# Optimization experiments

Measured on AMD Instinct MI355X. Metric: run time of the kernel, lower is better.

## Reference

```python
import jax, jax.numpy as jnp
import numpy as np

N = 1024
D_X = 128
D_Y = 128
NUM_STEPS = 200


def setup_inputs() -> dict:
    key = jax.random.key(0)
    k1, k2, k3, k4, k5 = jax.random.split(key, 5)
    init_samples_x = jax.random.normal(k1, (N, D_X), dtype=jnp.float32)
    init_samples_y = jax.random.normal(k2, (N, D_Y), dtype=jnp.float32)
    mean_final = jax.random.normal(k3, (D_X,), dtype=jnp.float32)
    # variance must be positive and bounded away from zero
    var_final = jax.random.uniform(k4, (D_X,), dtype=jnp.float32, minval=0.25, maxval=0.75)
    gammas = jnp.linspace(1e-3, 1e-2, NUM_STEPS, dtype=jnp.float32)
    # pre-generated per-step Gaussian noise (replaces torch.randn inside the loop)
    noise = jax.random.normal(k5, (NUM_STEPS, N, D_X), dtype=jnp.float32)
    return {
        "init_samples_x": init_samples_x,
        "init_samples_y": init_samples_y,
        "mean_final": mean_final,
        "var_final": var_final,
        "gammas": gammas,
        "noise": noise,
    }


def reference(init_samples_x, init_samples_y, mean_final, var_final, gammas, noise):
    """Faithful JAX port of Langevin.record_init_langevin.

    grad_gauss(x, m, v) = -(x - m) / v
    per step k:
        t_old = x + gamma_k * grad_gauss(x)
        x     = t_old + sqrt(2*gamma_k) * z_k
        t_new = x + gamma_k * grad_gauss(x)
        record x, y, t_old - t_new
    """
    num_steps = gammas.shape[0]
    n = init_samples_x.shape[0]

    def step(x, inp):
        gamma, z = inp
        t_old = x + gamma * (-(x - mean_final) / var_final)
        x_new = t_old + jnp.sqrt(2.0 * gamma) * z
        t_new = x_new + gamma * (-(x_new - mean_final) / var_final)
        return x_new, (x_new, t_old - t_new)

    _, (xs, outs) = jax.lax.scan(step, init_samples_x, (gammas, noise))
    # scan stacks along leading (step) axis -> [S, N, D]; match torch layout [N, S, D]
    x_tot = jnp.transpose(xs, (1, 0, 2))
    out = jnp.transpose(outs, (1, 0, 2))
    # y is constant across steps; the torch loop just replicates it
    y_tot = jnp.broadcast_to(init_samples_y[:, None, :], (n, num_steps, init_samples_y.shape[1]))
    steps_expanded = jnp.broadcast_to(
        jnp.arange(num_steps, dtype=jnp.int32)[None, :, None], (n, num_steps, 1)
    )
    return x_tot, y_tot, out, steps_expanded
```

## Files before the change

### kernel.cpp

```cpp
#include <hip/hip_runtime.h>
#include <math.h>

constexpr int N   = 1024;
constexpr int D   = 128;
constexpr int S   = 200;
constexpr int D2  = D / 2;
constexpr int ND2 = N * D2;
constexpr int CHAIN_BLOCKS = (N * D2) / 256;
constexpr int PF  = 8;

typedef float f2 __attribute__((ext_vector_type(2)));
typedef float f4 __attribute__((ext_vector_type(4)));

__global__ __launch_bounds__(256, 4) void langevin_kernel(
    const f2* __restrict__ x0,
    const f4* __restrict__ y0,
    const f2* __restrict__ mean,
    const f2* __restrict__ var,
    const float* __restrict__ gammas,
    const f2* __restrict__ noise,
    f2* __restrict__ x_tot,
    f4* __restrict__ y_tot,
    f2* __restrict__ outp,
    float* __restrict__ steps)
{
    if (blockIdx.x >= CHAIN_BLOCKS) {
        const int n   = blockIdx.x - CHAIN_BLOCKS;
        const int t   = threadIdx.x;
        const int col = t & 31;
        const int r0  = t >> 5;
        const f4  yv  = y0[(size_t)n * 32 + col];
        f4* yq = y_tot + (size_t)n * (S * 32);
        #pragma unroll
        for (int j = 0; j < S / 8; ++j) {
            const int k = r0 + j * 8;
            __builtin_nontemporal_store(yv, &yq[(size_t)k * 32 + col]);
        }
        if (t < S) steps[(size_t)n * S + t] = (float)t;
        return;
    }

    __shared__ float sg[S];
    __shared__ float ss[S];
    for (int i = threadIdx.x; i < S; i += 256) {
        float g = gammas[i];
        sg[i] = g;
        ss[i] = sqrtf(2.0f * g);
    }
    __syncthreads();

    const int idx = blockIdx.x * 256 + threadIdx.x;
    const int n   = idx >> 6;
    const int dp  = idx & 63;

    f2 x        = x0[idx];
    const f2 m  = mean[dp];
    const f2 v  = var[dp];
    const float ivx = 1.0f / v.x;
    const float ivy = 1.0f / v.y;

    const f2* zp = noise + idx;
    f2* xq = x_tot + (size_t)n * (S * D2) + dp;
    f2* oq = outp  + (size_t)n * (S * D2) + dp;

    f2 zb[PF];
    #pragma unroll
    for (int i = 0; i < PF; ++i)
        zb[i] = __builtin_nontemporal_load(&zp[(size_t)i * ND2]);

    #pragma unroll 1
    for (int kb = 0; kb < S; kb += PF) {
        f2 zn[PF];
        if (kb + PF < S) {
            #pragma unroll
            for (int i = 0; i < PF; ++i)
                zn[i] = __builtin_nontemporal_load(&zp[(size_t)(kb + PF + i) * ND2]);
        }
        #pragma unroll
        for (int i = 0; i < PF; ++i) {
            const int k = kb + i;
            const float g = sg[k];
            const float s = ss[k];
            const float gx = g * ivx;
            const float gy = g * ivy;

            const float tox = fmaf(-gx, x.x - m.x, x.x);
            const float toy = fmaf(-gy, x.y - m.y, x.y);
            x.x = fmaf(s, zb[i].x, tox);
            x.y = fmaf(s, zb[i].y, toy);
            const float tnx = fmaf(-gx, x.x - m.x, x.x);
            const float tny = fmaf(-gy, x.y - m.y, x.y);

            f2 o;
            o.x = tox - tnx;
            o.y = toy - tny;

            __builtin_nontemporal_store(x, &xq[(size_t)k * D2]);
            __builtin_nontemporal_store(o, &oq[(size_t)k * D2]);
        }
        #pragma unroll
        for (int i = 0; i < PF; ++i) zb[i] = zn[i];
    }
}

extern "C" void kernel_launch(void* const* d_in, const int* in_sizes, int n_in,
                              void* d_out, int out_size, void* d_ws, size_t ws_size,
                              hipStream_t stream)
{
    const float* x0     = (const float*)d_in[0];
    const float* y0     = (const float*)d_in[1];
    const float* mean   = (const float*)d_in[2];
    const float* var    = (const float*)d_in[3];
    const float* gammas = (const float*)d_in[4];
    const float* noise  = (const float*)d_in[5];

    float* x_tot = (float*)d_out;
    float* y_tot = x_tot + (size_t)N * S * D;
    float* outp  = y_tot + (size_t)N * S * D;
    float* steps = outp  + (size_t)N * S * D;

    dim3 grid(CHAIN_BLOCKS + N);
    dim3 block(256);
    langevin_kernel<<<grid, block, 0, stream>>>(
        (const f2*)x0, (const f4*)y0, (const f2*)mean,
        (const f2*)var, gammas, (const f2*)noise,
        (f2*)x_tot, (f4*)y_tot, (f2*)outp, steps);
}
```

Baseline: 396.6 us.

## Split time recurrence into segments via boundary precompute pass for more parallelism

Adds a first kernel that runs the x recurrence over all steps, reading the noise, and saves the state at seven segment boundaries into workspace. A second kernel then launches eight times as many chain blocks, each replaying one 25-step segment from its boundary state and writing x and the diff output. The aim is to expose more parallelism than the original 256 chain blocks, which run a serial 200-step loop. The cost is an extra kernel launch and a second full read of the noise tensor (about 105 MB). The original single kernel is kept as a fallback when the workspace is too small.

```diff
diff --git a/kernel.cpp b/kernel.cpp
--- a/kernel.cpp
+++ b/kernel.cpp
@@ -7,10 +7,165 @@
 constexpr int D2  = D / 2;
 constexpr int ND2 = N * D2;
 constexpr int CHAIN_BLOCKS = (N * D2) / 256;
+constexpr int SEG = 8;
+constexpr int L   = S / SEG;
+constexpr int PF1 = 10;
+constexpr int PF2 = 5;
 constexpr int PF  = 8;
 
 typedef float f2 __attribute__((ext_vector_type(2)));
 typedef float f4 __attribute__((ext_vector_type(4)));
+
+__global__ __launch_bounds__(256, 4) void boundary_kernel(
+    const f2* __restrict__ x0,
+    const f2* __restrict__ mean,
+    const f2* __restrict__ var,
+    const float* __restrict__ gammas,
+    const f2* __restrict__ noise,
+    f2* __restrict__ bnd)
+{
+    __shared__ float sg[S];
+    __shared__ float ss[S];
+    for (int i = threadIdx.x; i < S; i += 256) {
+        float g = gammas[i];
+        sg[i] = g;
+        ss[i] = sqrtf(2.0f * g);
+    }
+    __syncthreads();
+
+    const int idx = blockIdx.x * 256 + threadIdx.x;
+    const int dp  = idx & 63;
+
+    f2 x        = x0[idx];
+    const f2 m  = mean[dp];
+    const f2 v  = var[dp];
+    const float ivx = 1.0f / v.x;
+    const float ivy = 1.0f / v.y;
+
+    const f2* zp = noise + idx;
+
+    f2 zb[PF1];
+    #pragma unroll
+    for (int i = 0; i < PF1; ++i) zb[i] = zp[(size_t)i * ND2];
+
+    #pragma unroll 1
+    for (int kb = 0; kb < S; kb += PF1) {
+        f2 zn[PF1];
+        if (kb + PF1 < S) {
+            #pragma unroll
+            for (int i = 0; i < PF1; ++i)
+                zn[i] = zp[(size_t)(kb + PF1 + i) * ND2];
+        }
+        #pragma unroll
+        for (int i = 0; i < PF1; ++i) {
+            const int k = kb + i;
+            const float g = sg[k];
+            const float s = ss[k];
+            const float gx = g * ivx;
+            const float gy = g * ivy;
+            x.x = fmaf(s, zb[i].x, fmaf(-gx, x.x - m.x, x.x));
+            x.y = fmaf(s, zb[i].y, fmaf(-gy, x.y - m.y, x.y));
+            if (((k + 1) % L) == 0 && (k + 1) < S)
+                bnd[(size_t)((k + 1) / L - 1) * ND2 + idx] = x;
+        }
+        #pragma unroll
+        for (int i = 0; i < PF1; ++i) zb[i] = zn[i];
+    }
+}
+
+__global__ __launch_bounds__(256, 6) void segment_kernel(
+    const f2* __restrict__ x0,
+    const f4* __restrict__ y0,
+    const f2* __restrict__ mean,
+    const f2* __restrict__ var,
+    const float* __restrict__ gammas,
+    const f2* __restrict__ noise,
+    const f2* __restrict__ bnd,
+    f2* __restrict__ x_tot,
+    f4* __restrict__ y_tot,
+    f2* __restrict__ outp,
+    float* __restrict__ steps)
+{
+    if (blockIdx.x >= SEG * CHAIN_BLOCKS) {
+        const int n   = blockIdx.x - SEG * CHAIN_BLOCKS;
+        const int t   = threadIdx.x;
+        const int col = t & 31;
+        const int r0  = t >> 5;
+        const f4  yv  = y0[(size_t)n * 32 + col];
+        f4* yq = y_tot + (size_t)n * (S * 32);
+        #pragma unroll
+        for (int j = 0; j < S / 8; ++j) {
+            const int k = r0 + j * 8;
+            __builtin_nontemporal_store(yv, &yq[(size_t)k * 32 + col]);
+        }
+        if (t < S) steps[(size_t)n * S + t] = (float)t;
+        return;
+    }
+
+    __shared__ float sg[L];
+    __shared__ float ss[L];
+    const int seg = blockIdx.x / CHAIN_BLOCKS;
+    const int rb  = blockIdx.x % CHAIN_BLOCKS;
+    const int k0  = seg * L;
+    if (threadIdx.x < L) {
+        float g = gammas[k0 + threadIdx.x];
+        sg[threadIdx.x] = g;
+        ss[threadIdx.x] = sqrtf(2.0f * g);
+    }
+    __syncthreads();
+
+    const int idx = rb * 256 + threadIdx.x;
+    const int n   = idx >> 6;
+    const int dp  = idx & 63;
+
+    f2 x = (seg == 0) ? x0[idx] : bnd[(size_t)(seg - 1) * ND2 + idx];
+    const f2 m  = mean[dp];
+    const f2 v  = var[dp];
+    const float ivx = 1.0f / v.x;
+    const float ivy = 1.0f / v.y;
+
+    const f2* zp = noise + (size_t)k0 * ND2 + idx;
+    f2* xq = x_tot + (size_t)n * (S * D2) + (size_t)k0 * D2 + dp;
+    f2* oq = outp  + (size_t)n * (S * D2) + (size_t)k0 * D2 + dp;
+
+    f2 zb[PF2];
+    #pragma unroll
+    for (int i = 0; i < PF2; ++i) zb[i] = zp[(size_t)i * ND2];
+
+    #pragma unroll 1
+    for (int kb = 0; kb < L; kb += PF2) {
+        f2 zn[PF2];
+        if (kb + PF2 < L) {
+            #pragma unroll
+            for (int i = 0; i < PF2; ++i)
+                zn[i] = zp[(size_t)(kb + PF2 + i) * ND2];
+        }
+        #pragma unroll
+        for (int i = 0; i < PF2; ++i) {
+            const int k = kb + i;
+            const float g = sg[k];
+            const float s = ss[k];
+            const float gx = g * ivx;
+            const float gy = g * ivy;
+
+            const float tox = fmaf(-gx, x.x - m.x, x.x);
+            const float toy = fmaf(-gy, x.y - m.y, x.y);
+            x.x = fmaf(s, zb[i].x, tox);
+            x.y = fmaf(s, zb[i].y, toy);
+            const float tnx = fmaf(-gx, x.x - m.x, x.x);
+            const float tny = fmaf(-gy, x.y - m.y, x.y);
+
+            f2 o;
+            o.x = tox - tnx;
+            o.y = toy - tny;
+
+            __builtin_nontemporal_store(x, &xq[(size_t)k * D2]);
+            __builtin_nontemporal_store(o, &oq[(size_t)k * D2]);
+        }
+        #pragma unroll
+        for (int i = 0; i < PF2; ++i) zb[i] = zn[i];
+    }
+}
 
 __global__ __launch_bounds__(256, 4) void langevin_kernel(
     const f2* __restrict__ x0,
@@ -119,10 +274,19 @@
     float* outp  = y_tot + (size_t)N * S * D;
     float* steps = outp  + (size_t)N * S * D;
 
-    dim3 grid(CHAIN_BLOCKS + N);
-    dim3 block(256);
-    langevin_kernel<<<grid, block, 0, stream>>>(
-        (const f2*)x0, (const f4*)y0, (const f2*)mean,
-        (const f2*)var, gammas, (const f2*)noise,
-        (f2*)x_tot, (f4*)y_tot, (f2*)outp, steps);
-}
+    const size_t need = (size_t)(SEG - 1) * ND2 * sizeof(f2);
+    if (d_ws != nullptr && ws_size >= need) {
+        boundary_kernel<<<CHAIN_BLOCKS, 256, 0, stream>>>(
+            (const f2*)x0, (const f2*)mean, (const f2*)var, gammas,
+            (const f2*)noise, (f2*)d_ws);
+        segment_kernel<<<SEG * CHAIN_BLOCKS + N, 256, 0, stream>>>(
+            (const f2*)x0, (const f4*)y0, (const f2*)mean, (const f2*)var,
+            gammas, (const f2*)noise, (const f2*)d_ws,
+            (f2*)x_tot, (f4*)y_tot, (f2*)outp, steps);
+    } else {
+        langevin_kernel<<<CHAIN_BLOCKS + N, 256, 0, stream>>>(
+            (const f2*)x0, (const f4*)y0, (const f2*)mean, (const f2*)var,
+            gammas, (const f2*)noise,
+            (f2*)x_tot, (f4*)y_tot, (f2*)outp, steps);
+    }
+}
```

Result: no change. 399.6 us (+0.8%).

## Split Langevin chains into time segments with recomputed prefixes

Applied to the files above, without the earlier changes.

Each chain is split into 8 time segments handled by separate blocks. Each block replays the earlier steps, reading their noise without writing, to rebuild its starting state, then emits its own 25 steps. This raises the number of blocks working on the serial recurrence so the latency of one long chain no longer dominates. In exchange, total noise reads grow several-fold. Occupancy hint and prefetch depth are also changed.

```diff
diff --git a/kernel.cpp b/kernel.cpp
--- a/kernel.cpp
+++ b/kernel.cpp
@@ -7,12 +7,14 @@
 constexpr int D2  = D / 2;
 constexpr int ND2 = N * D2;
 constexpr int CHAIN_BLOCKS = (N * D2) / 256;
-constexpr int PF  = 8;
+constexpr int SEG = 8;
+constexpr int L   = S / SEG;
+constexpr int PF  = 5;
 
 typedef float f2 __attribute__((ext_vector_type(2)));
 typedef float f4 __attribute__((ext_vector_type(4)));
 
-__global__ __launch_bounds__(256, 4) void langevin_kernel(
+__global__ __launch_bounds__(256, 6) void langevin_seg_kernel(
     const f2* __restrict__ x0,
     const f4* __restrict__ y0,
     const f2* __restrict__ mean,
@@ -24,8 +26,8 @@
     f2* __restrict__ outp,
     float* __restrict__ steps)
 {
-    if (blockIdx.x >= CHAIN_BLOCKS) {
-        const int n   = blockIdx.x - CHAIN_BLOCKS;
+    if (blockIdx.x >= SEG * CHAIN_BLOCKS) {
+        const int n   = blockIdx.x - SEG * CHAIN_BLOCKS;
         const int t   = threadIdx.x;
         const int col = t & 31;
         const int r0  = t >> 5;
@@ -49,7 +51,11 @@
     }
     __syncthreads();
 
-    const int idx = blockIdx.x * 256 + threadIdx.x;
+    const int seg = blockIdx.x / CHAIN_BLOCKS;
+    const int rb  = blockIdx.x % CHAIN_BLOCKS;
+    const int k0  = seg * L;
+
+    const int idx = rb * 256 + threadIdx.x;
     const int n   = idx >> 6;
     const int dp  = idx & 63;
 
@@ -60,25 +66,47 @@
     const float ivy = 1.0f / v.y;
 
     const f2* zp = noise + idx;
-    f2* xq = x_tot + (size_t)n * (S * D2) + dp;
-    f2* oq = outp  + (size_t)n * (S * D2) + dp;
 
     f2 zb[PF];
     #pragma unroll
-    for (int i = 0; i < PF; ++i)
-        zb[i] = __builtin_nontemporal_load(&zp[(size_t)i * ND2]);
+    for (int i = 0; i < PF; ++i) zb[i] = zp[(size_t)i * ND2];
 
     #pragma unroll 1
-    for (int kb = 0; kb < S; kb += PF) {
+    for (int kb = 0; kb < k0; kb += PF) {
         f2 zn[PF];
-        if (kb + PF < S) {
-            #pragma unroll
-            for (int i = 0; i < PF; ++i)
-                zn[i] = __builtin_nontemporal_load(&zp[(size_t)(kb + PF + i) * ND2]);
-        }
+        #pragma unroll
+        for (int i = 0; i < PF; ++i)
+            zn[i] = zp[(size_t)(kb + PF + i) * ND2];
         #pragma unroll
         for (int i = 0; i < PF; ++i) {
             const int k = kb + i;
+            const float g = sg[k];
+            const float s = ss[k];
+            const float gx = g * ivx;
+            const float gy = g * ivy;
+            const float tox = fmaf(-gx, x.x - m.x, x.x);
+            const float toy = fmaf(-gy, x.y - m.y, x.y);
+            x.x = fmaf(s, zb[i].x, tox);
+            x.y = fmaf(s, zb[i].y, toy);
+        }
+        #pragma unroll
+        for (int i = 0; i < PF; ++i) zb[i] = zn[i];
+    }
+
+    const f2* zq = zp + (size_t)k0 * ND2;
+    f2* xq = x_tot + (size_t)n * (S * D2) + (size_t)k0 * D2 + dp;
+    f2* oq = outp  + (size_t)n * (S * D2) + (size_t)k0 * D2 + dp;
+
+    #pragma unroll 1
+    for (int kb = 0; kb < L; kb += PF) {
+        f2 zn[PF];
+        const bool more = (k0 + kb + PF) < S;
+        #pragma unroll
+        for (int i = 0; i < PF; ++i)
+            zn[i] = more ? zq[(size_t)(kb + PF + i) * ND2] : zb[i];
+        #pragma unroll
+        for (int i = 0; i < PF; ++i) {
+            const int k = k0 + kb + i;
             const float g = sg[k];
             const float s = ss[k];
             const float gx = g * ivx;
@@ -95,8 +123,8 @@
             o.x = tox - tnx;
             o.y = toy - tny;
 
-            __builtin_nontemporal_store(x, &xq[(size_t)k * D2]);
-            __builtin_nontemporal_store(o, &oq[(size_t)k * D2]);
+            __builtin_nontemporal_store(x, &xq[(size_t)(kb + i) * D2]);
+            __builtin_nontemporal_store(o, &oq[(size_t)(kb + i) * D2]);
         }
         #pragma unroll
         for (int i = 0; i < PF; ++i) zb[i] = zn[i];
@@ -119,10 +147,10 @@
     float* outp  = y_tot + (size_t)N * S * D;
     float* steps = outp  + (size_t)N * S * D;
 
-    dim3 grid(CHAIN_BLOCKS + N);
+    dim3 grid(SEG * CHAIN_BLOCKS + N);
     dim3 block(256);
-    langevin_kernel<<<grid, block, 0, stream>>>(
-        (const f2*)x0, (const f4*)y0, (const f2*)mean,
-        (const f2*)var, gammas, (const f2*)noise,
+    langevin_seg_kernel<<<grid, block, 0, stream>>>(
+        (const f2*)x0, (const f4*)y0, (const f2*)mean, (const f2*)var,
+        gammas, (const f2*)noise,
         (f2*)x_tot, (f4*)y_tot, (f2*)outp, steps);
 }
```

After: 423.9 us. 6.9% more time.
